# Kernel tuning notes

Hardware: AMD Instinct MI355X
Metric: run time of the kernel (lower is better)

Reference implementation:

```python
import jax, jax.numpy as jnp
import numpy as np

NUM_ROIS = 333
EPS = 1e-5
SLOPE = 0.3  # LeakyReLU negative slope
BATCH = 512


def _make_meta():
    rng = np.random.RandomState(42)
    sizes = rng.randint(100, 501, NUM_ROIS)          # per-ROI input voxels
    reduced = np.maximum(sizes // 8, 8)              # per-ROI reduced dim
    return sizes, reduced


def setup_inputs() -> dict:
    sizes, reduced = _make_meta()
    total = int(sizes.sum())
    max_in = int(sizes.max())
    max_out = int(reduced.max())
    in_off = np.concatenate([[0], np.cumsum(sizes)])[:-1]
    # gather index [R, max_in]; out-of-range slots point at a zero pad column (= total)
    k = np.arange(max_in)
    idx = np.where(k[None, :] < sizes[:, None], in_off[:, None] + k[None, :], total)
    # map concat positions -> flattened [R*max_out] positions (drops per-ROI padding)
    src_index = np.concatenate([r * max_out + np.arange(reduced[r]) for r in range(NUM_ROIS)])
    concat_dim = int(reduced.sum())

    key = jax.random.key(0)
    ks = jax.random.split(key, 12)
    x = jax.random.normal(ks[0], (BATCH, total), jnp.float32)
    W_enc = jax.random.normal(ks[1], (NUM_ROIS, max_out, max_in), jnp.float32) * 0.05
    b_enc = jax.random.normal(ks[2], (NUM_ROIS, max_out), jnp.float32) * 0.02
    gamma = 1.0 + 0.1 * jax.random.normal(ks[3], (NUM_ROIS, max_out), jnp.float32)
    beta = 0.1 * jax.random.normal(ks[4], (NUM_ROIS, max_out), jnp.float32)
    run_mean = 0.1 * jax.random.normal(ks[5], (NUM_ROIS, max_out), jnp.float32)
    run_var = jax.random.uniform(ks[6], (NUM_ROIS, max_out), jnp.float32, 0.5, 1.5)
    W_reg = jax.random.normal(ks[7], (300, concat_dim), jnp.float32) * 0.02
    b_reg = jax.random.normal(ks[8], (300,), jnp.float32) * 0.02
    W_cls = jax.random.normal(ks[9], (180, 300), jnp.float32) * 0.05
    b_cls = jax.random.normal(ks[10], (180,), jnp.float32) * 0.02
    return {
        'x': x, 'W_enc': W_enc, 'b_enc': b_enc, 'gamma': gamma, 'beta': beta,
        'run_mean': run_mean, 'run_var': run_var,
        'W_reg': W_reg, 'b_reg': b_reg, 'W_cls': W_cls, 'b_cls': b_cls,
        'idx': jnp.asarray(idx, jnp.int32), 'src_index': jnp.asarray(src_index, jnp.int32),
    }


def reference(x, W_enc, b_enc, gamma, beta, run_mean, run_var,
              W_reg, b_reg, W_cls, b_cls, idx, src_index):
    B = x.shape[0]
    # pad a zero column so ragged gather lands on zeros; padded weight cols hit zeros
    x_pad = jnp.concatenate([x, jnp.zeros((B, 1), x.dtype)], axis=1)
    g = x_pad[:, idx]                                   # [B, R, max_in]
    z = jnp.einsum('brk,rok->bro', g, W_enc) + b_enc    # grouped GEMM: [B, R, max_out]
    # BatchNorm1d (inference form with running stats) + LeakyReLU(0.3)
    y = gamma * (z - run_mean) * jax.lax.rsqrt(run_var + EPS) + beta
    y = jnp.where(y > 0, y, SLOPE * y)
    concat_out = y.reshape(B, -1)[:, src_index]         # [B, concat_dim] (drop ROI padding)
    reg_out = concat_out @ W_reg.T + b_reg              # dropout is identity in eval
    y_pred = jax.nn.softmax(reg_out @ W_cls.T + b_cls, axis=-1)
    return concat_out, reg_out, y_pred
```

## Files before the change

kernel.cpp:

```cpp
#include <hip/hip_runtime.h>
#include <hip/hip_bf16.h>

#define NROIS 333
#define BATCH 512
#define NREG 300
#define NCLS 180
#define EPSV 1e-5f
#define SLOPEV 0.3f

typedef __attribute__((ext_vector_type(8))) short bf16x8;
typedef __attribute__((ext_vector_type(4))) float f32x4;

static __device__ __forceinline__ bf16x8 pack8(const float v[8]) {
  union { bf16x8 o; __hip_bfloat16 h[8]; } u;
  #pragma unroll
  for (int e = 0; e < 8; e++) u.h[e] = __float2bfloat16(v[e]);
  return u.o;
}

__global__ void meta_kernel(const int* __restrict__ idx, const int* __restrict__ src,
                            int* __restrict__ meta, int max_in, int max_out,
                            int total, int concat_dim) {
  int r = blockIdx.x * blockDim.x + threadIdx.x;
  if (r >= NROIS) return;
  const int* row = idx + (long)r * max_in;
  int in_off = row[0];
  int lo = 0, hi = max_in;
  while (lo < hi) { int mid = (lo + hi) >> 1; if (row[mid] < total) lo = mid + 1; else hi = mid; }
  int size = lo;
  int t1 = r * max_out;
  lo = 0; hi = concat_dim;
  while (lo < hi) { int mid = (lo + hi) >> 1; if (src[mid] < t1) lo = mid + 1; else hi = mid; }
  int out_off = lo;
  int t2 = t1 + max_out;
  hi = concat_dim;
  while (lo < hi) { int mid = (lo + hi) >> 1; if (src[mid] < t2) lo = mid + 1; else hi = mid; }
  meta[r] = in_off;
  meta[NROIS + r] = size;
  meta[2 * NROIS + r] = out_off;
  meta[3 * NROIS + r] = lo - out_off;
}

__global__ void init_reg_kernel(const float* __restrict__ b_reg, float* __restrict__ reg_out) {
  int i = blockIdx.x * blockDim.x + threadIdx.x;
  if (i < BATCH * NREG) reg_out[i] = b_reg[i % NREG];
}

__global__ __launch_bounds__(256) void transcode_kernel(
    const float* __restrict__ concat, const float* __restrict__ W_reg,
    __hip_bfloat16* __restrict__ cbf, __hip_bfloat16* __restrict__ wbf,
    int cd, int cdp) {
  int row = blockIdx.x;
  const float* src;
  __hip_bfloat16* dst;
  if (row < BATCH) { src = concat + (long)row * cd; dst = cbf + (long)row * cdp; }
  else             { src = W_reg + (long)(row - BATCH) * cd; dst = wbf + (long)(row - BATCH) * cdp; }
  for (int k = threadIdx.x * 8; k < cdp; k += 256 * 8) {
    if (k + 8 <= cd) {
      float4 a = *(const float4*)(src + k), b = *(const float4*)(src + k + 4);
      float v[8] = {a.x, a.y, a.z, a.w, b.x, b.y, b.z, b.w};
      *(bf16x8*)(dst + k) = pack8(v);
    } else {
      for (int e = 0; e < 8 && k + e < cdp; e++)
        dst[k + e] = __float2bfloat16((k + e < cd) ? src[k + e] : 0.f);
    }
  }
}

__global__ __launch_bounds__(256) void enc_kernel(
    const float* __restrict__ x,
    const float* __restrict__ W_enc,
    const float* __restrict__ b_enc,
    const float* __restrict__ gamma,
    const float* __restrict__ beta,
    const float* __restrict__ run_mean,
    const float* __restrict__ run_var,
    const int* __restrict__ meta,
    float* __restrict__ concat_out,
    int total, int max_in, int max_out, int concat_dim) {
  int r = blockIdx.x;
  int b0 = blockIdx.y * 128;
  int in_off  = meta[r];
  int size    = meta[NROIS + r];
  int out_off = meta[2 * NROIS + r];
  int red     = meta[3 * NROIS + r];
  int ntiles  = (red + 15) >> 4;

  __shared__ __hip_bfloat16 xs[2][128][40];
  __shared__ __hip_bfloat16 wsh[2][64][40];

  int t = threadIdx.x;
  int row0 = t >> 2, chk = t & 3;
  const float* xg0 = x + (long)(b0 + row0) * total + in_off;
  long xstride = (long)64 * total;
  int wrow = (row0 < red) ? row0 : (red - 1);
  const float* wg0 = W_enc + ((long)r * max_out + wrow) * max_in;

  int w = t >> 6, l = t & 63, lq = l >> 4, lm = l & 15;

  f32x4 acc[2][4];
  #pragma unroll
  for (int i = 0; i < 2; i++)
    #pragma unroll
    for (int nb = 0; nb < 4; nb++) acc[i][nb] = (f32x4){0.f, 0.f, 0.f, 0.f};

  int nsteps = (size + 31) >> 5;
  float xr[2][8], wr[8];

  auto load_regs = [&](int kb) {
    int k0 = kb + chk * 8;
    if (k0 + 8 <= size) {
      #pragma unroll
      for (int s = 0; s < 2; s++) {
        const float* p = xg0 + (long)s * xstride + k0;
        float4 a = *(const float4*)p, b = *(const float4*)(p + 4);
        xr[s][0]=a.x; xr[s][1]=a.y; xr[s][2]=a.z; xr[s][3]=a.w;
        xr[s][4]=b.x; xr[s][5]=b.y; xr[s][6]=b.z; xr[s][7]=b.w;
      }
      const float* p = wg0 + k0;
      float4 a = *(const float4*)p, b = *(const float4*)(p + 4);
      wr[0]=a.x; wr[1]=a.y; wr[2]=a.z; wr[3]=a.w;
      wr[4]=b.x; wr[5]=b.y; wr[6]=b.z; wr[7]=b.w;
    } else {
      #pragma unroll
      for (int s = 0; s < 2; s++)
        #pragma unroll
        for (int e = 0; e < 8; e++)
          xr[s][e] = (k0 + e < size) ? xg0[(long)s * xstride + k0 + e] : 0.f;
      #pragma unroll
      for (int e = 0; e < 8; e++)
        wr[e] = (k0 + e < size) ? wg0[k0 + e] : 0.f;
    }
  };
  auto write_lds = [&](int buf) {
    #pragma unroll
    for (int s = 0; s < 2; s++)
      *(bf16x8*)&xs[buf][row0 + 64 * s][chk * 8] = pack8(xr[s]);
    *(bf16x8*)&wsh[buf][row0][chk * 8] = pack8(wr);
  };

  load_regs(0);
  write_lds(0);
  __syncthreads();

  for (int s = 0; s < nsteps; s++) {
    int buf = s & 1;
    bool more = (s + 1 < nsteps);
    if (more) load_regs((s + 1) * 32);
    bf16x8 af[2];
    #pragma unroll
    for (int i = 0; i < 2; i++)
      af[i] = *(const bf16x8*)&xs[buf][32 * w + 16 * i + lm][lq * 8];
    for (int nb = 0; nb < ntiles; nb++) {
      bf16x8 bfr = *(const bf16x8*)&wsh[buf][16 * nb + lm][lq * 8];
      #pragma unroll
      for (int i = 0; i < 2; i++)
        acc[i][nb] = __builtin_amdgcn_mfma_f32_16x16x32_bf16(af[i], bfr, acc[i][nb], 0, 0, 0);
    }
    if (more) write_lds(buf ^ 1);
    __syncthreads();
  }

  long base = (long)r * max_out;
  for (int nb = 0; nb < ntiles; nb++) {
    int oc = nb * 16 + lm;
    if (oc < red) {
      float sc  = gamma[base + oc] * rsqrtf(run_var[base + oc] + EPSV);
      float off = beta[base + oc] + sc * (b_enc[base + oc] - run_mean[base + oc]);
      #pragma unroll
      for (int i = 0; i < 2; i++) {
        #pragma unroll
        for (int j = 0; j < 4; j++) {
          int br = b0 + 32 * w + 16 * i + lq * 4 + j;
          float y = sc * acc[i][nb][j] + off;
          y = (y > 0.f) ? y : SLOPEV * y;
          concat_out[(long)br * concat_dim + out_off + oc] = y;
        }
      }
    }
  }
}

template <bool BF>
__global__ __launch_bounds__(256) void reg_kernel(
    const void* __restrict__ Asrc, const void* __restrict__ Bsrc,
    float* __restrict__ reg_out, int cd, int astride, int span) {
  int j0 = blockIdx.x * 64;
  int b0 = blockIdx.y * 128;
  int kstart = blockIdx.z * span;
  int kend = min(kstart + span, cd);
  if (kstart >= kend) return;
  int ntiles = min(4, (NREG - j0 + 15) >> 4);

  __shared__ __hip_bfloat16 as_[2][128][40];
  __shared__ __hip_bfloat16 bs_[2][64][40];

  int t = threadIdx.x;
  int row0 = t >> 2, chk = t & 3;
  int jr = j0 + row0;
  int bj = (jr < NREG) ? jr : (NREG - 1);
  const __hip_bfloat16* aB = (const __hip_bfloat16*)Asrc + (long)(b0 + row0) * astride + kstart;
  const __hip_bfloat16* bB = (const __hip_bfloat16*)Bsrc + (long)bj * astride + kstart;
  const float* aF = (const float*)Asrc + (long)(b0 + row0) * astride + kstart;
  const float* bF = (const float*)Bsrc + (long)bj * astride + kstart;
  long astr = (long)64 * astride;
  int klen = kend - kstart;

  int w = t >> 6, l = t & 63, lq = l >> 4, lm = l & 15;

  f32x4 acc[2][4];
  #pragma unroll
  for (int i = 0; i < 2; i++)
    #pragma unroll
    for (int nb = 0; nb < 4; nb++) acc[i][nb] = (f32x4){0.f, 0.f, 0.f, 0.f};

  int nsteps = (klen + 31) >> 5;
  bf16x8 arv[2], brv;
  float arf[2][8], brf[8];

  auto load_regs = [&](int kb) {
    int k0 = kb + chk * 8;
    if (k0 + 8 <= klen) {
      if (BF) {
        #pragma unroll
        for (int s = 0; s < 2; s++) arv[s] = *(const bf16x8*)(aB + (long)s * astr + k0);
        brv = *(const bf16x8*)(bB + k0);
      } else {
        #pragma unroll
        for (int s = 0; s < 2; s++) {
          const float* p = aF + (long)s * astr + k0;
          float4 a = *(const float4*)p, b = *(const float4*)(p + 4);
          arf[s][0]=a.x; arf[s][1]=a.y; arf[s][2]=a.z; arf[s][3]=a.w;
          arf[s][4]=b.x; arf[s][5]=b.y; arf[s][6]=b.z; arf[s][7]=b.w;
        }
        const float* p = bF + k0;
        float4 a = *(const float4*)p, b = *(const float4*)(p + 4);
        brf[0]=a.x; brf[1]=a.y; brf[2]=a.z; brf[3]=a.w;
        brf[4]=b.x; brf[5]=b.y; brf[6]=b.z; brf[7]=b.w;
      }
    } else {
      union { bf16x8 v; __hip_bfloat16 h[8]; } ua[2], ub;
      #pragma unroll
      for (int s = 0; s < 2; s++)
        #pragma unroll
        for (int e = 0; e < 8; e++) {
          bool in = (k0 + e < klen);
          if (BF) ua[s].h[e] = in ? aB[(long)s * astr + k0 + e] : __float2bfloat16(0.f);
          else    arf[s][e] = in ? aF[(long)s * astr + k0 + e] : 0.f;
        }
      #pragma unroll
      for (int e = 0; e < 8; e++) {
        bool in = (k0 + e < klen);
        if (BF) ub.h[e] = in ? bB[k0 + e] : __float2bfloat16(0.f);
        else    brf[e] = in ? bF[k0 + e] : 0.f;
      }
      if (BF) { arv[0] = ua[0].v; arv[1] = ua[1].v; brv = ub.v; }
    }
  };
  auto write_lds = [&](int buf) {
    #pragma unroll
    for (int s = 0; s < 2; s++)
      *(bf16x8*)&as_[buf][row0 + 64 * s][chk * 8] = BF ? arv[s] : pack8(arf[s]);
    *(bf16x8*)&bs_[buf][row0][chk * 8] = BF ? brv : pack8(brf);
  };

  load_regs(0);
  write_lds(0);
  __syncthreads();

  for (int s = 0; s < nsteps; s++) {
    int buf = s & 1;
    bool more = (s + 1 < nsteps);
    if (more) load_regs((s + 1) * 32);
    bf16x8 af[2];
    #pragma unroll
    for (int i = 0; i < 2; i++)
      af[i] = *(const bf16x8*)&as_[buf][32 * w + 16 * i + lm][lq * 8];
    for (int nb = 0; nb < ntiles; nb++) {
      bf16x8 bfr = *(const bf16x8*)&bs_[buf][16 * nb + lm][lq * 8];
      #pragma unroll
      for (int i = 0; i < 2; i++)
        acc[i][nb] = __builtin_amdgcn_mfma_f32_16x16x32_bf16(af[i], bfr, acc[i][nb], 0, 0, 0);
    }
    if (more) write_lds(buf ^ 1);
    __syncthreads();
  }

  for (int nb = 0; nb < ntiles; nb++) {
    int j = j0 + nb * 16 + lm;
    if (j < NREG) {
      #pragma unroll
      for (int i = 0; i < 2; i++)
        #pragma unroll
        for (int jj = 0; jj < 4; jj++) {
          int br2 = b0 + 32 * w + 16 * i + lq * 4 + jj;
          atomicAdd(&reg_out[(long)br2 * NREG + j], acc[i][nb][jj]);
        }
    }
  }
}

__global__ __launch_bounds__(192) void cls_kernel(
    const float* __restrict__ reg_out,
    const float* __restrict__ W_cls,
    const float* __restrict__ b_cls,
    float* __restrict__ cls_out) {
  int b = blockIdx.x;
  int t = threadIdx.x;
  __shared__ __align__(16) float rrow[NREG];
  __shared__ float lm[3];
  for (int iB = t; iB < NREG; iB += 192) rrow[iB] = reg_out[(long)b * NREG + iB];
  __syncthreads();
  float s = 0.f;
  if (t < NCLS) {
    s = b_cls[t];
    const float4* wr  = (const float4*)(W_cls + (long)t * NREG);
    const float4* rr4 = (const float4*)rrow;
    #pragma unroll 5
    for (int i = 0; i < NREG / 4; ++i) {
      float4 wv = wr[i], rv = rr4[i];
      s += wv.x * rv.x + wv.y * rv.y + wv.z * rv.z + wv.w * rv.w;
    }
  }
  float v = (t < NCLS) ? s : -3.4e38f;
  #pragma unroll
  for (int o = 32; o > 0; o >>= 1) v = fmaxf(v, __shfl_xor(v, o, 64));
  if ((t & 63) == 0) lm[t >> 6] = v;
  __syncthreads();
  float bmax = fmaxf(fmaxf(lm[0], lm[1]), lm[2]);
  __syncthreads();
  float e = (t < NCLS) ? __expf(s - bmax) : 0.f;
  float ss = e;
  #pragma unroll
  for (int o = 32; o > 0; o >>= 1) ss += __shfl_xor(ss, o, 64);
  if ((t & 63) == 0) lm[t >> 6] = ss;
  __syncthreads();
  float bsum = lm[0] + lm[1] + lm[2];
  if (t < NCLS) cls_out[(long)b * NCLS + t] = e / bsum;
}

extern "C" void kernel_launch(void* const* d_in, const int* in_sizes, int n_in,
                              void* d_out, int out_size, void* d_ws, size_t ws_size,
                              hipStream_t stream) {
  const float* x     = (const float*)d_in[0];
  const float* W_enc = (const float*)d_in[1];
  const float* b_enc = (const float*)d_in[2];
  const float* gam   = (const float*)d_in[3];
  const float* bet   = (const float*)d_in[4];
  const float* rmean = (const float*)d_in[5];
  const float* rvar  = (const float*)d_in[6];
  const float* W_reg = (const float*)d_in[7];
  const float* b_reg = (const float*)d_in[8];
  const float* W_cls = (const float*)d_in[9];
  const float* b_cls = (const float*)d_in[10];
  const int* idx = (const int*)d_in[11];
  const int* src = (const int*)d_in[12];

  int total      = in_sizes[0] / BATCH;
  int max_out    = in_sizes[2] / NROIS;
  int max_in     = in_sizes[11] / NROIS;
  int concat_dim = in_sizes[12];
  int cdp        = (concat_dim + 7) & ~7;

  int* meta = (int*)d_ws;
  size_t bf_off = 8192;
  size_t cbf_bytes = (size_t)BATCH * cdp * sizeof(__hip_bfloat16);
  size_t wbf_bytes = (size_t)NREG * cdp * sizeof(__hip_bfloat16);
  int use_bf = (ws_size >= bf_off + cbf_bytes + wbf_bytes) ? 1 : 0;
  __hip_bfloat16* cbf = (__hip_bfloat16*)((char*)d_ws + bf_off);
  __hip_bfloat16* wbf = (__hip_bfloat16*)((char*)d_ws + bf_off + cbf_bytes);

  float* out_concat = (float*)d_out;
  float* out_reg = out_concat + (long)BATCH * concat_dim;
  float* out_cls = out_reg + (long)BATCH * NREG;

  meta_kernel<<<dim3((NROIS + 255) / 256), 256, 0, stream>>>(idx, src, meta, max_in, max_out, total, concat_dim);
  init_reg_kernel<<<dim3((BATCH * NREG + 255) / 256), 256, 0, stream>>>(b_reg, out_reg);
  enc_kernel<<<dim3(NROIS, BATCH / 128), 256, 0, stream>>>(x, W_enc, b_enc, gam, bet, rmean, rvar,
                                                           meta, out_concat, total, max_in, max_out, concat_dim);
  const int SPLIT = 32;
  int span = ((concat_dim + SPLIT * 32 - 1) / (SPLIT * 32)) * 32;
  dim3 rgrid((NREG + 63) / 64, BATCH / 128, SPLIT);
  if (use_bf) {
    transcode_kernel<<<BATCH + NREG, 256, 0, stream>>>(out_concat, W_reg, cbf, wbf, concat_dim, cdp);
    reg_kernel<true><<<rgrid, 256, 0, stream>>>(cbf, wbf, out_reg, concat_dim, cdp, span);
  } else {
    reg_kernel<false><<<rgrid, 256, 0, stream>>>(out_concat, W_reg, out_reg, concat_dim, concat_dim, span);
  }
  cls_kernel<<<BATCH, 192, 0, stream>>>(out_reg, W_cls, b_cls, out_cls);
}
```

Before: 473.4 us.

## Deepen register prefetch to two stages and use lightweight LDS-only barrier

Both the encoder grouped GEMM and the regression GEMM kernels now keep two register sets of global loads in flight, issuing loads two k-steps ahead instead of one. This hides more global-memory latency behind the MFMA work. The __syncthreads is also replaced with an inline-asm s_waitcnt lgkmcnt(0) + s_barrier, which does not wait on outstanding global loads. Together these let prefetches stay outstanding across barriers, at the cost of more registers and some risk of lower occupancy. Register sets are indexed by a runtime parity, so the compiler may spill them to scratch.

```diff
diff --git a/kernel.cpp b/kernel.cpp
--- a/kernel.cpp
+++ b/kernel.cpp
@@ -10,6 +10,10 @@
 
 typedef __attribute__((ext_vector_type(8))) short bf16x8;
 typedef __attribute__((ext_vector_type(4))) float f32x4;
+
+static __device__ __forceinline__ void block_sync_lds() {
+  asm volatile("s_waitcnt lgkmcnt(0)\n\ts_barrier" ::: "memory");
+}
 
 static __device__ __forceinline__ bf16x8 pack8(const float v[8]) {
   union { bf16x8 o; __hip_bfloat16 h[8]; } u;
@@ -105,48 +109,48 @@
     for (int nb = 0; nb < 4; nb++) acc[i][nb] = (f32x4){0.f, 0.f, 0.f, 0.f};
 
   int nsteps = (size + 31) >> 5;
-  float xr[2][8], wr[8];
-
-  auto load_regs = [&](int kb) {
+  float xr[2][2][8], wr[2][8];
+
+  auto load_regs = [&](int set, int kb) {
     int k0 = kb + chk * 8;
     if (k0 + 8 <= size) {
       #pragma unroll
       for (int s = 0; s < 2; s++) {
         const float* p = xg0 + (long)s * xstride + k0;
         float4 a = *(const float4*)p, b = *(const float4*)(p + 4);
-        xr[s][0]=a.x; xr[s][1]=a.y; xr[s][2]=a.z; xr[s][3]=a.w;
-        xr[s][4]=b.x; xr[s][5]=b.y; xr[s][6]=b.z; xr[s][7]=b.w;
+        xr[set][s][0]=a.x; xr[set][s][1]=a.y; xr[set][s][2]=a.z; xr[set][s][3]=a.w;
+        xr[set][s][4]=b.x; xr[set][s][5]=b.y; xr[set][s][6]=b.z; xr[set][s][7]=b.w;
       }
       const float* p = wg0 + k0;
       float4 a = *(const float4*)p, b = *(const float4*)(p + 4);
-      wr[0]=a.x; wr[1]=a.y; wr[2]=a.z; wr[3]=a.w;
-      wr[4]=b.x; wr[5]=b.y; wr[6]=b.z; wr[7]=b.w;
+      wr[set][0]=a.x; wr[set][1]=a.y; wr[set][2]=a.z; wr[set][3]=a.w;
+      wr[set][4]=b.x; wr[set][5]=b.y; wr[set][6]=b.z; wr[set][7]=b.w;
     } else {
       #pragma unroll
       for (int s = 0; s < 2; s++)
         #pragma unroll
         for (int e = 0; e < 8; e++)
-          xr[s][e] = (k0 + e < size) ? xg0[(long)s * xstride + k0 + e] : 0.f;
+          xr[set][s][e] = (k0 + e < size) ? xg0[(long)s * xstride + k0 + e] : 0.f;
       #pragma unroll
       for (int e = 0; e < 8; e++)
-        wr[e] = (k0 + e < size) ? wg0[k0 + e] : 0.f;
+        wr[set][e] = (k0 + e < size) ? wg0[k0 + e] : 0.f;
     }
   };
-  auto write_lds = [&](int buf) {
+  auto write_lds = [&](int buf, int set) {
     #pragma unroll
     for (int s = 0; s < 2; s++)
-      *(bf16x8*)&xs[buf][row0 + 64 * s][chk * 8] = pack8(xr[s]);
-    *(bf16x8*)&wsh[buf][row0][chk * 8] = pack8(wr);
+      *(bf16x8*)&xs[buf][row0 + 64 * s][chk * 8] = pack8(xr[set][s]);
+    *(bf16x8*)&wsh[buf][row0][chk * 8] = pack8(wr[set]);
   };
 
-  load_regs(0);
-  write_lds(0);
-  __syncthreads();
+  load_regs(0, 0);
+  if (nsteps > 1) load_regs(1, 32);
+  write_lds(0, 0);
+  block_sync_lds();
 
   for (int s = 0; s < nsteps; s++) {
     int buf = s & 1;
-    bool more = (s + 1 < nsteps);
-    if (more) load_regs((s + 1) * 32);
+    if (s + 2 < nsteps) load_regs(s & 1, (s + 2) * 32);
     bf16x8 af[2];
     #pragma unroll
     for (int i = 0; i < 2; i++)
@@ -157,8 +161,8 @@
       for (int i = 0; i < 2; i++)
         acc[i][nb] = __builtin_amdgcn_mfma_f32_16x16x32_bf16(af[i], bfr, acc[i][nb], 0, 0, 0);
     }
-    if (more) write_lds(buf ^ 1);
-    __syncthreads();
+    if (s + 1 < nsteps) write_lds(buf ^ 1, (s + 1) & 1);
+    block_sync_lds();
   }
 
   long base = (long)r * max_out;
@@ -215,28 +219,28 @@
     for (int nb = 0; nb < 4; nb++) acc[i][nb] = (f32x4){0.f, 0.f, 0.f, 0.f};
 
   int nsteps = (klen + 31) >> 5;
-  bf16x8 arv[2], brv;
-  float arf[2][8], brf[8];
-
-  auto load_regs = [&](int kb) {
+  bf16x8 arv[2][2], brv[2];
+  float arf[2][2][8], brf[2][8];
+
+  auto load_regs = [&](int set, int kb) {
     int k0 = kb + chk * 8;
     if (k0 + 8 <= klen) {
       if (BF) {
         #pragma unroll
-        for (int s = 0; s < 2; s++) arv[s] = *(const bf16x8*)(aB + (long)s * astr + k0);
-        brv = *(const bf16x8*)(bB + k0);
+        for (int s = 0; s < 2; s++) arv[set][s] = *(const bf16x8*)(aB + (long)s * astr + k0);
+        brv[set] = *(const bf16x8*)(bB + k0);
       } else {
         #pragma unroll
         for (int s = 0; s < 2; s++) {
           const float* p = aF + (long)s * astr + k0;
           float4 a = *(const float4*)p, b = *(const float4*)(p + 4);
-          arf[s][0]=a.x; arf[s][1]=a.y; arf[s][2]=a.z; arf[s][3]=a.w;
-          arf[s][4]=b.x; arf[s][5]=b.y; arf[s][6]=b.z; arf[s][7]=b.w;
+          arf[set][s][0]=a.x; arf[set][s][1]=a.y; arf[set][s][2]=a.z; arf[set][s][3]=a.w;
+          arf[set][s][4]=b.x; arf[set][s][5]=b.y; arf[set][s][6]=b.z; arf[set][s][7]=b.w;
         }
         const float* p = bF + k0;
         float4 a = *(const float4*)p, b = *(const float4*)(p + 4);
-        brf[0]=a.x; brf[1]=a.y; brf[2]=a.z; brf[3]=a.w;
-        brf[4]=b.x; brf[5]=b.y; brf[6]=b.z; brf[7]=b.w;
+        brf[set][0]=a.x; brf[set][1]=a.y; brf[set][2]=a.z; brf[set][3]=a.w;
+        brf[set][4]=b.x; brf[set][5]=b.y; brf[set][6]=b.z; brf[set][7]=b.w;
       }
     } else {
       union { bf16x8 v; __hip_bfloat16 h[8]; } ua[2], ub;
@@ -246,32 +250,32 @@
         for (int e = 0; e < 8; e++) {
           bool in = (k0 + e < klen);
           if (BF) ua[s].h[e] = in ? aB[(long)s * astr + k0 + e] : __float2bfloat16(0.f);
-          else    arf[s][e] = in ? aF[(long)s * astr + k0 + e] : 0.f;
+          else    arf[set][s][e] = in ? aF[(long)s * astr + k0 + e] : 0.f;
         }
       #pragma unroll
       for (int e = 0; e < 8; e++) {
         bool in = (k0 + e < klen);
         if (BF) ub.h[e] = in ? bB[k0 + e] : __float2bfloat16(0.f);
-        else    brf[e] = in ? bF[k0 + e] : 0.f;
+        else    brf[set][e] = in ? bF[k0 + e] : 0.f;
       }
-      if (BF) { arv[0] = ua[0].v; arv[1] = ua[1].v; brv = ub.v; }
+      if (BF) { arv[set][0] = ua[0].v; arv[set][1] = ua[1].v; brv[set] = ub.v; }
     }
   };
-  auto write_lds = [&](int buf) {
+  auto write_lds = [&](int buf, int set) {
     #pragma unroll
     for (int s = 0; s < 2; s++)
-      *(bf16x8*)&as_[buf][row0 + 64 * s][chk * 8] = BF ? arv[s] : pack8(arf[s]);
-    *(bf16x8*)&bs_[buf][row0][chk * 8] = BF ? brv : pack8(brf);
+      *(bf16x8*)&as_[buf][row0 + 64 * s][chk * 8] = BF ? arv[set][s] : pack8(arf[set][s]);
+    *(bf16x8*)&bs_[buf][row0][chk * 8] = BF ? brv[set] : pack8(brf[set]);
   };
 
-  load_regs(0);
-  write_lds(0);
-  __syncthreads();
+  load_regs(0, 0);
+  if (nsteps > 1) load_regs(1, 32);
+  write_lds(0, 0);
+  block_sync_lds();
 
   for (int s = 0; s < nsteps; s++) {
     int buf = s & 1;
-    bool more = (s + 1 < nsteps);
-    if (more) load_regs((s + 1) * 32);
+    if (s + 2 < nsteps) load_regs(s & 1, (s + 2) * 32);
     bf16x8 af[2];
     #pragma unroll
     for (int i = 0; i < 2; i++)
@@ -282,8 +286,8 @@
       for (int i = 0; i < 2; i++)
         acc[i][nb] = __builtin_amdgcn_mfma_f32_16x16x32_bf16(af[i], bfr, acc[i][nb], 0, 0, 0);
     }
-    if (more) write_lds(buf ^ 1);
-    __syncthreads();
+    if (s + 1 < nsteps) write_lds(buf ^ 1, (s + 1) & 1);
+    block_sync_lds();
   }
 
   for (int nb = 0; nb < ntiles; nb++) {
```

After: 764.1 us. 61.4% more time.
